# Kernel tuning notes

Hardware: AMD Instinct MI355X
Metric: run time of the kernel (lower is better)

## Reference

```python
import jax, jax.numpy as jnp
import numpy as np

B, H, S, D = 2, 12, 2048, 64


def setup_inputs() -> dict:
    key = jax.random.key(0)
    kq, kk, kv = jax.random.split(key, 3)
    q = jax.random.normal(kq, (B, H, S, D), dtype=jnp.float32)
    k = jax.random.normal(kk, (B, H, S, D), dtype=jnp.float32)
    v = jax.random.normal(kv, (B, H, S, D), dtype=jnp.float32)
    mask = jnp.zeros((1, 1, S, S), dtype=jnp.float32)  # additive mask
    return {"q": q, "k": k, "v": v, "mask": mask}


def reference(q, k, v, mask):
    # scaled dot-product attention, materializing full [B,H,S,S] weights
    dk = jnp.sqrt(jnp.asarray(q.shape[-1], dtype=q.dtype))
    logits = jnp.einsum("bhsd,bhtd->bhst", q, k) / dk
    logits = logits + mask  # additive mask, broadcast over B,H
    we = jax.nn.softmax(logits, axis=-1)
    out = jnp.einsum("bhst,bhtd->bhsd", we, v)
    return (out, we)
```

## Files before the change

### kernel.cpp

```cpp
#include <hip/hip_runtime.h>


typedef short          s16x8 __attribute__((ext_vector_type(8)));
typedef unsigned short u16x8 __attribute__((ext_vector_type(8)));
typedef unsigned short u16x4 __attribute__((ext_vector_type(4)));
typedef float          f32x4 __attribute__((ext_vector_type(4)));

#define kS   2048
#define kD   64
#define kBH  24
#define OUT_ELEMS (kBH * kS * kD)

static __device__ __forceinline__ unsigned short f2bf(float f) {
    union { float f; unsigned u; } x; x.f = f;
    return (unsigned short)((x.u + 0x7fffu + ((x.u >> 16) & 1u)) >> 16);
}

static __device__ __forceinline__ u16x8 cvt8(const float4 f0, const float4 f1) {
    u16x8 r;
    r[0] = f2bf(f0.x); r[1] = f2bf(f0.y); r[2] = f2bf(f0.z); r[3] = f2bf(f0.w);
    r[4] = f2bf(f1.x); r[5] = f2bf(f1.y); r[6] = f2bf(f1.z); r[7] = f2bf(f1.w);
    return r;
}

__global__ __launch_bounds__(256)
void attn_fused(const float* __restrict__ Qg, const float* __restrict__ Kg,
                const float* __restrict__ Vg, const float* __restrict__ Mg,
                float* __restrict__ Og, float* __restrict__ Wg)
{
    __shared__ __align__(16) unsigned short k_sh[2][32 * 64];
    __shared__ __align__(16) unsigned short vt_sh[2][64 * 32];
    __shared__ __align__(16) unsigned short p_sh[4][16 * 40];

    const int tid  = threadIdx.x;
    const int wv   = tid >> 6;
    const int lane = tid & 63;
    const int g    = lane >> 4;
    const int c    = lane & 15;

    const int wg = ((int)blockIdx.x & 7) * 96 + ((int)blockIdx.x >> 3);
    const int bh = wg >> 5;
    const int qb = wg & 31;
    const int q0 = qb * 64 + wv * 16;

    s16x8 aQ[2];
    {
        const float* qp = Qg + ((size_t)(bh * kS + q0 + c)) * kD + g * 8;
        #pragma unroll
        for (int h = 0; h < 2; ++h) {
            float4 f0 = *(const float4*)(qp + h * 32);
            float4 f1 = *(const float4*)(qp + h * 32 + 4);
            union { u16x8 u; s16x8 s; } t; t.u = cvt8(f0, f1);
            aQ[h] = t.s;
        }
    }

    const int sr = tid >> 3;
    const int sc = (tid & 7) * 8;
    const float* kstage = Kg + ((size_t)bh * kS + sr) * kD + sc;
    const float* vstage = Vg + ((size_t)bh * kS + sr) * kD + sc;
    const unsigned kaddr_w = (unsigned)((sr * 128 + sc * 2) ^ ((sr & 7) << 4));
    const float* mrow = Mg + (size_t)(q0 + g * 4) * kS;

    {
        *(u16x8*)((char*)k_sh[0] + kaddr_w) = cvt8(*(const float4*)kstage, *(const float4*)(kstage + 4));
    }
    __syncthreads();

    float sm[4] = {0.f, 0.f, 0.f, 0.f};
    int cur = 0;
    for (int t0 = 0; t0 < kS; t0 += 32) {
        const bool nxt = (t0 + 32) < kS;
        float4 kf0, kf1;
        if (nxt) {
            const float* src = kstage + (size_t)(t0 + 32) * kD;
            kf0 = *(const float4*)src; kf1 = *(const float4*)(src + 4);
        }
        #pragma unroll
        for (int tt = 0; tt < 2; ++tt) {
            const int row = tt * 16 + c;
            f32x4 acc = {0.f, 0.f, 0.f, 0.f};
            #pragma unroll
            for (int h = 0; h < 2; ++h) {
                const unsigned a = (unsigned)((row * 128 + h * 64 + g * 16) ^ ((row & 7) << 4));
                s16x8 bK = *(const s16x8*)((const char*)k_sh[cur] + a);
                acc = __builtin_amdgcn_mfma_f32_16x16x32_bf16(aQ[h], bK, acc, 0, 0, 0);
            }
            const int t = t0 + tt * 16 + c;
            #pragma unroll
            for (int j = 0; j < 4; ++j)
                sm[j] += __expf(acc[j] * 0.125f + mrow[(size_t)j * kS + t]);
        }
        if (nxt) {
            *(u16x8*)((char*)k_sh[cur ^ 1] + kaddr_w) = cvt8(kf0, kf1);
            __syncthreads();
            cur ^= 1;
        }
    }
    #pragma unroll
    for (int j = 0; j < 4; ++j) {
        float s = sm[j];
        s += __shfl_xor(s, 1);
        s += __shfl_xor(s, 2);
        s += __shfl_xor(s, 4);
        s += __shfl_xor(s, 8);
        sm[j] = 1.0f / s;
    }

    f32x4 accO[4];
    #pragma unroll
    for (int dt = 0; dt < 4; ++dt) accO[dt] = f32x4{0.f, 0.f, 0.f, 0.f};

    __syncthreads();
    {
        *(u16x8*)((char*)k_sh[0] + kaddr_w) = cvt8(*(const float4*)kstage, *(const float4*)(kstage + 4));
        u16x8 vb = cvt8(*(const float4*)vstage, *(const float4*)(vstage + 4));
        #pragma unroll
        for (int i = 0; i < 8; ++i) {
            const int d = sc + i;
            const unsigned b = (unsigned)((d * 64 + sr * 2) ^ (((d >> 3) & 7) << 4));
            *(unsigned short*)((char*)vt_sh[0] + b) = vb[i];
        }
    }
    __syncthreads();

    const int wr = lane >> 3;
    const int wcb = lane & 7;
    float* wbase = Wg + ((size_t)(bh * kS + q0)) * kS;

    cur = 0;
    for (int t0 = 0; t0 < kS; t0 += 32) {
        const bool nxt = (t0 + 32) < kS;
        float4 kf0, kf1, vf0, vf1;
        if (nxt) {
            const float* srck = kstage + (size_t)(t0 + 32) * kD;
            kf0 = *(const float4*)srck; kf1 = *(const float4*)(srck + 4);
            const float* srcv = vstage + (size_t)(t0 + 32) * kD;
            vf0 = *(const float4*)srcv; vf1 = *(const float4*)(srcv + 4);
        }

        #pragma unroll
        for (int tt = 0; tt < 2; ++tt) {
            const int row = tt * 16 + c;
            f32x4 acc = {0.f, 0.f, 0.f, 0.f};
            #pragma unroll
            for (int h = 0; h < 2; ++h) {
                const unsigned a = (unsigned)((row * 128 + h * 64 + g * 16) ^ ((row & 7) << 4));
                s16x8 bK = *(const s16x8*)((const char*)k_sh[cur] + a);
                acc = __builtin_amdgcn_mfma_f32_16x16x32_bf16(aQ[h], bK, acc, 0, 0, 0);
            }
            const int t = t0 + tt * 16 + c;
            #pragma unroll
            for (int j = 0; j < 4; ++j) {
                const float p = __expf(acc[j] * 0.125f + mrow[(size_t)j * kS + t]) * sm[j];
                p_sh[wv][(g * 4 + j) * 40 + tt * 16 + c] = f2bf(p);
            }
        }

        s16x8 pa = *(const s16x8*)((const char*)&p_sh[wv][0] + c * 80 + g * 16);
        #pragma unroll
        for (int dt = 0; dt < 4; ++dt) {
            const int d = dt * 16 + c;
            const unsigned b = (unsigned)((d * 64 + g * 16) ^ (((d >> 3) & 7) << 4));
            s16x8 bV = *(const s16x8*)((const char*)vt_sh[cur] + b);
            accO[dt] = __builtin_amdgcn_mfma_f32_16x16x32_bf16(pa, bV, accO[dt], 0, 0, 0);
        }

        #pragma unroll
        for (int s = 0; s < 2; ++s) {
            const int row = wr + s * 8;
            u16x4 pb = *(const u16x4*)((const char*)&p_sh[wv][0] + row * 80 + wcb * 8);
            f32x4 w;
            #pragma unroll
            for (int i = 0; i < 4; ++i) {
                union { unsigned u; float f; } x; x.u = ((unsigned)pb[i]) << 16;
                w[i] = x.f;
            }
            __builtin_nontemporal_store(w, (f32x4*)(wbase + (size_t)row * kS + t0 + wcb * 4));
        }

        if (nxt) {
            *(u16x8*)((char*)k_sh[cur ^ 1] + kaddr_w) = cvt8(kf0, kf1);
            u16x8 vb = cvt8(vf0, vf1);
            #pragma unroll
            for (int i = 0; i < 8; ++i) {
                const int d = sc + i;
                const unsigned b = (unsigned)((d * 64 + sr * 2) ^ (((d >> 3) & 7) << 4));
                *(unsigned short*)((char*)vt_sh[cur ^ 1] + b) = vb[i];
            }
            __syncthreads();
            cur ^= 1;
        }
    }

    float* orow = Og + ((size_t)(bh * kS + q0 + g * 4)) * kD + c;
    #pragma unroll
    for (int dt = 0; dt < 4; ++dt) {
        #pragma unroll
        for (int j = 0; j < 4; ++j)
            __builtin_nontemporal_store(accO[dt][j], orow + (size_t)j * kD + dt * 16);
    }
}

extern "C" void kernel_launch(void* const* d_in, const int* in_sizes, int n_in,
                              void* d_out, int out_size, void* d_ws, size_t ws_size,
                              hipStream_t stream) {
    const float* q = (const float*)d_in[0];
    const float* k = (const float*)d_in[1];
    const float* v = (const float*)d_in[2];
    const float* m = (const float*)d_in[3];
    float* out = (float*)d_out;
    float* we  = out + OUT_ELEMS;
    attn_fused<<<dim3(kBH * 32), dim3(256), 0, stream>>>(q, k, v, m, out, we);
}
```

Measured before the change: 152.6 us.

## Pre-convert K, V and mask to bf16 in a separate pass before attention

Adds a conversion kernel that writes K, V and the mask as bf16 into workspace. The main attention kernel then reads bf16 directly, which halves the global reads of K/V, which are re-read by every query block across two passes, and of the mask. It also drops the in-loop conversion ALU work. The cost is an extra launch plus a full pass over K, V and the 4M-element mask. The mask is now rounded to bf16, and an fp32 fallback runs when the workspace is too small.

```diff
diff --git a/kernel.cpp b/kernel.cpp
--- a/kernel.cpp
+++ b/kernel.cpp
@@ -10,12 +10,17 @@
 #define kD   64
 #define kBH  24
 #define OUT_ELEMS (kBH * kS * kD)
+#define MASK_ELEMS (kS * kS)
+#define CVT_TOTAL (2 * OUT_ELEMS + MASK_ELEMS)
 
 static __device__ __forceinline__ unsigned short f2bf(float f) {
     union { float f; unsigned u; } x; x.f = f;
     return (unsigned short)((x.u + 0x7fffu + ((x.u >> 16) & 1u)) >> 16);
 }
-
+static __device__ __forceinline__ float bf2f(unsigned short v) {
+    union { unsigned u; float f; } x; x.u = ((unsigned)v) << 16;
+    return x.f;
+}
 static __device__ __forceinline__ u16x8 cvt8(const float4 f0, const float4 f1) {
     u16x8 r;
     r[0] = f2bf(f0.x); r[1] = f2bf(f0.y); r[2] = f2bf(f0.z); r[3] = f2bf(f0.w);
@@ -24,9 +29,25 @@
 }
 
 __global__ __launch_bounds__(256)
-void attn_fused(const float* __restrict__ Qg, const float* __restrict__ Kg,
-                const float* __restrict__ Vg, const float* __restrict__ Mg,
-                float* __restrict__ Og, float* __restrict__ Wg)
+void cvt_bf16(const float* __restrict__ K, const float* __restrict__ V,
+              const float* __restrict__ M, unsigned short* __restrict__ W)
+{
+    const size_t e = ((size_t)blockIdx.x * 256 + threadIdx.x) * 8;
+    if (e >= CVT_TOTAL) return;
+    const float* src;
+    size_t off;
+    if (e < OUT_ELEMS)            { src = K; off = e; }
+    else if (e < 2 * OUT_ELEMS)   { src = V; off = e - OUT_ELEMS; }
+    else                          { src = M; off = e - 2 * OUT_ELEMS; }
+    float4 a = *(const float4*)(src + off);
+    float4 b = *(const float4*)(src + off + 4);
+    *(u16x8*)(W + e) = cvt8(a, b);
+}
+
+__global__ __launch_bounds__(256)
+void attn_fused_b(const float* __restrict__ Qg, const unsigned short* __restrict__ Kb,
+                  const unsigned short* __restrict__ Vb, const unsigned short* __restrict__ Mb,
+                  float* __restrict__ Og, float* __restrict__ Wg)
 {
     __shared__ __align__(16) unsigned short k_sh[2][32 * 64];
     __shared__ __align__(16) unsigned short vt_sh[2][64 * 32];
@@ -57,13 +78,13 @@
 
     const int sr = tid >> 3;
     const int sc = (tid & 7) * 8;
-    const float* kstage = Kg + ((size_t)bh * kS + sr) * kD + sc;
-    const float* vstage = Vg + ((size_t)bh * kS + sr) * kD + sc;
+    const unsigned short* kstage = Kb + ((size_t)bh * kS + sr) * kD + sc;
+    const unsigned short* vstage = Vb + ((size_t)bh * kS + sr) * kD + sc;
     const unsigned kaddr_w = (unsigned)((sr * 128 + sc * 2) ^ ((sr & 7) << 4));
-    const float* mrow = Mg + (size_t)(q0 + g * 4) * kS;
-
-    {
-        *(u16x8*)((char*)k_sh[0] + kaddr_w) = cvt8(*(const float4*)kstage, *(const float4*)(kstage + 4));
+    const unsigned short* mrow = Mb + (size_t)(q0 + g * 4) * kS;
+
+    {
+        *(u16x8*)((char*)k_sh[0] + kaddr_w) = *(const u16x8*)kstage;
     }
     __syncthreads();
 
@@ -71,11 +92,8 @@
     int cur = 0;
     for (int t0 = 0; t0 < kS; t0 += 32) {
         const bool nxt = (t0 + 32) < kS;
-        float4 kf0, kf1;
-        if (nxt) {
-            const float* src = kstage + (size_t)(t0 + 32) * kD;
-            kf0 = *(const float4*)src; kf1 = *(const float4*)(src + 4);
-        }
+        u16x8 kf;
+        if (nxt) kf = *(const u16x8*)(kstage + (size_t)(t0 + 32) * kD);
         #pragma unroll
         for (int tt = 0; tt < 2; ++tt) {
             const int row = tt * 16 + c;
@@ -89,10 +107,10 @@
             const int t = t0 + tt * 16 + c;
             #pragma unroll
             for (int j = 0; j < 4; ++j)
-                sm[j] += __expf(acc[j] * 0.125f + mrow[(size_t)j * kS + t]);
-        }
-        if (nxt) {
-            *(u16x8*)((char*)k_sh[cur ^ 1] + kaddr_w) = cvt8(kf0, kf1);
+                sm[j] += __expf(acc[j] * 0.125f + bf2f(mrow[(size_t)j * kS + t]));
+        }
+        if (nxt) {
+            *(u16x8*)((char*)k_sh[cur ^ 1] + kaddr_w) = kf;
             __syncthreads();
             cur ^= 1;
         }
@@ -113,8 +131,8 @@
 
     __syncthreads();
     {
-        *(u16x8*)((char*)k_sh[0] + kaddr_w) = cvt8(*(const float4*)kstage, *(const float4*)(kstage + 4));
-        u16x8 vb = cvt8(*(const float4*)vstage, *(const float4*)(vstage + 4));
+        *(u16x8*)((char*)k_sh[0] + kaddr_w) = *(const u16x8*)kstage;
+        u16x8 vb = *(const u16x8*)vstage;
         #pragma unroll
         for (int i = 0; i < 8; ++i) {
             const int d = sc + i;
@@ -131,12 +149,10 @@
     cur = 0;
     for (int t0 = 0; t0 < kS; t0 += 32) {
         const bool nxt = (t0 + 32) < kS;
-        float4 kf0, kf1, vf0, vf1;
-        if (nxt) {
-            const float* srck = kstage + (size_t)(t0 + 32) * kD;
-            kf0 = *(const float4*)srck; kf1 = *(const float4*)(srck + 4);
-            const float* srcv = vstage + (size_t)(t0 + 32) * kD;
-            vf0 = *(const float4*)srcv; vf1 = *(const float4*)(srcv + 4);
+        u16x8 kf, vf;
+        if (nxt) {
+            kf = *(const u16x8*)(kstage + (size_t)(t0 + 32) * kD);
+            vf = *(const u16x8*)(vstage + (size_t)(t0 + 32) * kD);
         }
 
         #pragma unroll
@@ -152,7 +168,7 @@
             const int t = t0 + tt * 16 + c;
             #pragma unroll
             for (int j = 0; j < 4; ++j) {
-                const float p = __expf(acc[j] * 0.125f + mrow[(size_t)j * kS + t]) * sm[j];
+                const float p = __expf(acc[j] * 0.125f + bf2f(mrow[(size_t)j * kS + t])) * sm[j];
                 p_sh[wv][(g * 4 + j) * 40 + tt * 16 + c] = f2bf(p);
             }
         }
@@ -172,10 +188,181 @@
             u16x4 pb = *(const u16x4*)((const char*)&p_sh[wv][0] + row * 80 + wcb * 8);
             f32x4 w;
             #pragma unroll
-            for (int i = 0; i < 4; ++i) {
-                union { unsigned u; float f; } x; x.u = ((unsigned)pb[i]) << 16;
-                w[i] = x.f;
-            }
+            for (int i = 0; i < 4; ++i) w[i] = bf2f(pb[i]);
+            __builtin_nontemporal_store(w, (f32x4*)(wbase + (size_t)row * kS + t0 + wcb * 4));
+        }
+
+        if (nxt) {
+            *(u16x8*)((char*)k_sh[cur ^ 1] + kaddr_w) = kf;
+            #pragma unroll
+            for (int i = 0; i < 8; ++i) {
+                const int d = sc + i;
+                const unsigned b = (unsigned)((d * 64 + sr * 2) ^ (((d >> 3) & 7) << 4));
+                *(unsigned short*)((char*)vt_sh[cur ^ 1] + b) = vf[i];
+            }
+            __syncthreads();
+            cur ^= 1;
+        }
+    }
+
+    float* orow = Og + ((size_t)(bh * kS + q0 + g * 4)) * kD + c;
+    #pragma unroll
+    for (int dt = 0; dt < 4; ++dt) {
+        #pragma unroll
+        for (int j = 0; j < 4; ++j)
+            __builtin_nontemporal_store(accO[dt][j], orow + (size_t)j * kD + dt * 16);
+    }
+}
+
+__global__ __launch_bounds__(256)
+void attn_fused_f32(const float* __restrict__ Qg, const float* __restrict__ Kg,
+                    const float* __restrict__ Vg, const float* __restrict__ Mg,
+                    float* __restrict__ Og, float* __restrict__ Wg)
+{
+    __shared__ __align__(16) unsigned short k_sh[2][32 * 64];
+    __shared__ __align__(16) unsigned short vt_sh[2][64 * 32];
+    __shared__ __align__(16) unsigned short p_sh[4][16 * 40];
+
+    const int tid  = threadIdx.x;
+    const int wv   = tid >> 6;
+    const int lane = tid & 63;
+    const int g    = lane >> 4;
+    const int c    = lane & 15;
+
+    const int wg = ((int)blockIdx.x & 7) * 96 + ((int)blockIdx.x >> 3);
+    const int bh = wg >> 5;
+    const int qb = wg & 31;
+    const int q0 = qb * 64 + wv * 16;
+
+    s16x8 aQ[2];
+    {
+        const float* qp = Qg + ((size_t)(bh * kS + q0 + c)) * kD + g * 8;
+        #pragma unroll
+        for (int h = 0; h < 2; ++h) {
+            float4 f0 = *(const float4*)(qp + h * 32);
+            float4 f1 = *(const float4*)(qp + h * 32 + 4);
+            union { u16x8 u; s16x8 s; } t; t.u = cvt8(f0, f1);
+            aQ[h] = t.s;
+        }
+    }
+
+    const int sr = tid >> 3;
+    const int sc = (tid & 7) * 8;
+    const float* kstage = Kg + ((size_t)bh * kS + sr) * kD + sc;
+    const float* vstage = Vg + ((size_t)bh * kS + sr) * kD + sc;
+    const unsigned kaddr_w = (unsigned)((sr * 128 + sc * 2) ^ ((sr & 7) << 4));
+    const float* mrow = Mg + (size_t)(q0 + g * 4) * kS;
+
+    {
+        *(u16x8*)((char*)k_sh[0] + kaddr_w) = cvt8(*(const float4*)kstage, *(const float4*)(kstage + 4));
+    }
+    __syncthreads();
+
+    float sm[4] = {0.f, 0.f, 0.f, 0.f};
+    int cur = 0;
+    for (int t0 = 0; t0 < kS; t0 += 32) {
+        const bool nxt = (t0 + 32) < kS;
+        float4 kf0, kf1;
+        if (nxt) {
+            const float* src = kstage + (size_t)(t0 + 32) * kD;
+            kf0 = *(const float4*)src; kf1 = *(const float4*)(src + 4);
+        }
+        #pragma unroll
+        for (int tt = 0; tt < 2; ++tt) {
+            const int row = tt * 16 + c;
+            f32x4 acc = {0.f, 0.f, 0.f, 0.f};
+            #pragma unroll
+            for (int h = 0; h < 2; ++h) {
+                const unsigned a = (unsigned)((row * 128 + h * 64 + g * 16) ^ ((row & 7) << 4));
+                s16x8 bK = *(const s16x8*)((const char*)k_sh[cur] + a);
+                acc = __builtin_amdgcn_mfma_f32_16x16x32_bf16(aQ[h], bK, acc, 0, 0, 0);
+            }
+            const int t = t0 + tt * 16 + c;
+            #pragma unroll
+            for (int j = 0; j < 4; ++j)
+                sm[j] += __expf(acc[j] * 0.125f + mrow[(size_t)j * kS + t]);
+        }
+        if (nxt) {
+            *(u16x8*)((char*)k_sh[cur ^ 1] + kaddr_w) = cvt8(kf0, kf1);
+            __syncthreads();
+            cur ^= 1;
+        }
+    }
+    #pragma unroll
+    for (int j = 0; j < 4; ++j) {
+        float s = sm[j];
+        s += __shfl_xor(s, 1);
+        s += __shfl_xor(s, 2);
+        s += __shfl_xor(s, 4);
+        s += __shfl_xor(s, 8);
+        sm[j] = 1.0f / s;
+    }
+
+    f32x4 accO[4];
+    #pragma unroll
+    for (int dt = 0; dt < 4; ++dt) accO[dt] = f32x4{0.f, 0.f, 0.f, 0.f};
+
+    __syncthreads();
+    {
+        *(u16x8*)((char*)k_sh[0] + kaddr_w) = cvt8(*(const float4*)kstage, *(const float4*)(kstage + 4));
+        u16x8 vb = cvt8(*(const float4*)vstage, *(const float4*)(vstage + 4));
+        #pragma unroll
+        for (int i = 0; i < 8; ++i) {
+            const int d = sc + i;
+            const unsigned b = (unsigned)((d * 64 + sr * 2) ^ (((d >> 3) & 7) << 4));
+            *(unsigned short*)((char*)vt_sh[0] + b) = vb[i];
+        }
+    }
+    __syncthreads();
+
+    const int wr = lane >> 3;
+    const int wcb = lane & 7;
+    float* wbase = Wg + ((size_t)(bh * kS + q0)) * kS;
+
+    cur = 0;
+    for (int t0 = 0; t0 < kS; t0 += 32) {
+        const bool nxt = (t0 + 32) < kS;
+        float4 kf0, kf1, vf0, vf1;
+        if (nxt) {
+            const float* srck = kstage + (size_t)(t0 + 32) * kD;
+            kf0 = *(const float4*)srck; kf1 = *(const float4*)(srck + 4);
+            const float* srcv = vstage + (size_t)(t0 + 32) * kD;
+            vf0 = *(const float4*)srcv; vf1 = *(const float4*)(srcv + 4);
+        }
+        #pragma unroll
+        for (int tt = 0; tt < 2; ++tt) {
+            const int row = tt * 16 + c;
+            f32x4 acc = {0.f, 0.f, 0.f, 0.f};
+            #pragma unroll
+            for (int h = 0; h < 2; ++h) {
+                const unsigned a = (unsigned)((row * 128 + h * 64 + g * 16) ^ ((row & 7) << 4));
+                s16x8 bK = *(const s16x8*)((const char*)k_sh[cur] + a);
+                acc = __builtin_amdgcn_mfma_f32_16x16x32_bf16(aQ[h], bK, acc, 0, 0, 0);
+            }
+            const int t = t0 + tt * 16 + c;
+            #pragma unroll
+            for (int j = 0; j < 4; ++j) {
+                const float p = __expf(acc[j] * 0.125f + mrow[(size_t)j * kS + t]) * sm[j];
+                p_sh[wv][(g * 4 + j) * 40 + tt * 16 + c] = f2bf(p);
+            }
+        }
+
+        s16x8 pa = *(const s16x8*)((const char*)&p_sh[wv][0] + c * 80 + g * 16);
+        #pragma unroll
+        for (int dt = 0; dt < 4; ++dt) {
+            const int d = dt * 16 + c;
+            const unsigned b = (unsigned)((d * 64 + g * 16) ^ (((d >> 3) & 7) << 4));
+            s16x8 bV = *(const s16x8*)((const char*)vt_sh[cur] + b);
+            accO[dt] = __builtin_amdgcn_mfma_f32_16x16x32_bf16(pa, bV, accO[dt], 0, 0, 0);
+        }
+
+        #pragma unroll
+        for (int s = 0; s < 2; ++s) {
+            const int row = wr + s * 8;
+            u16x4 pb = *(const u16x4*)((const char*)&p_sh[wv][0] + row * 80 + wcb * 8);
+            f32x4 w;
+            #pragma unroll
+            for (int i = 0; i < 4; ++i) w[i] = bf2f(pb[i]);
             __builtin_nontemporal_store(w, (f32x4*)(wbase + (size_t)row * kS + t0 + wcb * 4));
         }
 
@@ -211,5 +398,14 @@
     const float* m = (const float*)d_in[3];
     float* out = (float*)d_out;
     float* we  = out + OUT_ELEMS;
-    attn_fused<<<dim3(kBH * 32), dim3(256), 0, stream>>>(q, k, v, m, out, we);
-}
+
+    const size_t need = (size_t)CVT_TOTAL * sizeof(unsigned short);
+    if (ws_size >= need) {
+        unsigned short* wsb = (unsigned short*)d_ws;
+        cvt_bf16<<<dim3(CVT_TOTAL / 8 / 256), dim3(256), 0, stream>>>(k, v, m, wsb);
+        attn_fused_b<<<dim3(kBH * 32), dim3(256), 0, stream>>>(
+            q, wsb, wsb + OUT_ELEMS, wsb + 2 * OUT_ELEMS, out, we);
+    } else {
+        attn_fused_f32<<<dim3(kBH * 32), dim3(256), 0, stream>>>(q, k, v, m, out, we);
+    }
+}
```

Result: faster. 143.8 us (-5.8%).
